# Kernel optimization log

Measured on AMD Instinct MI355X. Metric: run time of the kernel, lower is better.

Reference implementation:

```python
import jax, jax.numpy as jnp
import numpy as np

N_TOKENS = 8192
D_MODEL = 1024
D_HIDDEN = 2 * D_MODEL
N_EXPERTS = 16
TOP_K = 2


def setup_inputs() -> dict:
    key = jax.random.key(0)
    ks = jax.random.split(key, 6)
    s_in = 1.0 / np.sqrt(D_MODEL)
    s_hid = 1.0 / np.sqrt(D_HIDDEN)
    return {
        "x": jax.random.normal(ks[0], (N_TOKENS, D_MODEL), dtype=jnp.float32),
        # gate: Linear(d_model, n_experts, bias=False); stored as [E, d] like torch weight
        "Wg": jax.random.uniform(ks[1], (N_EXPERTS, D_MODEL), jnp.float32, -s_in, s_in),
        # per-expert MLP params, stacked on leading expert axis; W laid out [in, out]
        "W1": jax.random.uniform(ks[2], (N_EXPERTS, D_MODEL, D_HIDDEN), jnp.float32, -s_in, s_in),
        "b1": jax.random.uniform(ks[3], (N_EXPERTS, D_HIDDEN), jnp.float32, -s_in, s_in),
        "W2": jax.random.uniform(ks[4], (N_EXPERTS, D_HIDDEN, D_MODEL), jnp.float32, -s_hid, s_hid),
        "b2": jax.random.uniform(ks[5], (N_EXPERTS, D_MODEL), jnp.float32, -s_hid, s_hid),
    }


def reference(x, Wg, W1, b1, W2, b2):
    # Router: top-k logits, softmax over the k selected logits (in fp32)
    logits = x @ Wg.T                                  # [N, E]
    topk_vals, topk_idx = jax.lax.top_k(logits, TOP_K)  # [N, K]
    rw = jax.nn.softmax(topk_vals.astype(jnp.float32), axis=-1).astype(x.dtype)
    # Combine top-k weights into per-(token, expert) weights [N, E]
    cw = (jax.nn.one_hot(topk_idx, N_EXPERTS, dtype=x.dtype) * rw[..., None]).sum(axis=1)
    # Dense per-expert MLP, weighted combine (equivalent to gather/scatter index_add_)
    out = jnp.zeros_like(x)
    for e in range(N_EXPERTS):
        h = jax.nn.relu(x @ W1[e] + b1[e])             # [N, D_HIDDEN]
        out = out + (h @ W2[e] + b2[e]) * cw[:, e:e + 1]
    return out
```

## Files before the change

kernel.cpp:

```cpp
#include <hip/hip_runtime.h>
#include <hip/hip_bf16.h>
#include <stdint.h>

#define NTOK 8192
#define DM   1024
#define DH   2048
#define NE   16

#define NWRK  768
#define QCAP1 2048
#define QCAP2 1024

typedef float  f32x4  __attribute__((ext_vector_type(4)));
typedef __bf16 bf16x8 __attribute__((ext_vector_type(8)));

__device__ __forceinline__ unsigned short f2bf(float f) {
  union { __bf16 b; unsigned short u; } c; c.b = (__bf16)f; return c.u;
}

__device__ __forceinline__ void glds16(const void* g, void* l) {
  __builtin_amdgcn_global_load_lds(
      (const __attribute__((address_space(1))) void*)g,
      (__attribute__((address_space(3))) void*)l, 16, 0, 0);
}

__global__ __launch_bounds__(256) void router_kernel(
    const float* __restrict__ x, const float* __restrict__ Wg,
    unsigned short* __restrict__ xb, int* __restrict__ eidx,
    float* __restrict__ ewt, float* __restrict__ outz)
{
  const int lane = threadIdx.x & 63;
  const int wave = threadIdx.x >> 6;
  const int t = blockIdx.x * 4 + wave;
  const float* xr = x + (size_t)t * DM;

  float4 xv[4];
#pragma unroll
  for (int c = 0; c < 4; ++c)
    xv[c] = *(const float4*)(xr + c * 256 + lane * 4);

  unsigned short* xbr = xb + (size_t)t * DM;
#pragma unroll
  for (int c = 0; c < 4; ++c) {
    ushort4 u;
    u.x = f2bf(xv[c].x); u.y = f2bf(xv[c].y);
    u.z = f2bf(xv[c].z); u.w = f2bf(xv[c].w);
    *(ushort4*)(xbr + c * 256 + lane * 4) = u;
  }

  {
    float4 z4 = {0.f, 0.f, 0.f, 0.f};
    float* orow = outz + (size_t)t * DM;
#pragma unroll
    for (int c = 0; c < 4; ++c)
      *(float4*)(orow + c * 256 + lane * 4) = z4;
  }

  float acc[NE];
#pragma unroll
  for (int e = 0; e < NE; ++e) acc[e] = 0.f;
#pragma unroll
  for (int e = 0; e < NE; ++e) {
#pragma unroll
    for (int c = 0; c < 4; ++c) {
      float4 wv = *(const float4*)(Wg + e * DM + c * 256 + lane * 4);
      acc[e] += xv[c].x * wv.x + xv[c].y * wv.y + xv[c].z * wv.z + xv[c].w * wv.w;
    }
  }
#pragma unroll
  for (int e = 0; e < NE; ++e) {
    float v = acc[e];
    v += __shfl_xor(v, 1);  v += __shfl_xor(v, 2);  v += __shfl_xor(v, 4);
    v += __shfl_xor(v, 8);  v += __shfl_xor(v, 16); v += __shfl_xor(v, 32);
    acc[e] = v;
  }
  if (lane == 0) {
    float v0 = -1e30f; int i0 = 0;
#pragma unroll
    for (int e = 0; e < NE; ++e) if (acc[e] > v0) { v0 = acc[e]; i0 = e; }
    float v1 = -1e30f; int i1 = 0;
#pragma unroll
    for (int e = 0; e < NE; ++e) if (e != i0 && acc[e] > v1) { v1 = acc[e]; i1 = e; }
    float p = expf(v1 - v0);
    float s = 1.f / (1.f + p);
    eidx[2 * t] = i0; eidx[2 * t + 1] = i1;
    ewt[2 * t] = s;   ewt[2 * t + 1] = p * s;
  }
}

__global__ __launch_bounds__(1024) void planprep_kernel(
    const int* __restrict__ eidx, const float* __restrict__ ewt,
    int* __restrict__ cnt, int* __restrict__ offv,
    int* __restrict__ tok, float* __restrict__ wtl,
    int* __restrict__ wl1, int* __restrict__ wl2,
    int* __restrict__ qn1, int* __restrict__ qn2,
    int* __restrict__ qc1, int* __restrict__ qc2,
    const float* __restrict__ W1, unsigned short* __restrict__ w1t,
    const float* __restrict__ W2, unsigned short* __restrict__ w2t)
{
  __shared__ float t[4][64][68];
  __shared__ int wcnt[16][NE];
  __shared__ int wbase[16][NE];
  __shared__ int offs[NE];
  __shared__ int s_nmt[NE];
  __shared__ int s_pnmt[NE + 1];

  if (blockIdx.x != 0) {
    const int idx = blockIdx.x - 1;
    const int tg  = threadIdx.x >> 8;
    const int t8  = threadIdx.x & 255;
    const float* W; unsigned short* WT; int K, N, tt, bx, by;
    if (idx < 2048) {
      W = W1; WT = w1t; K = DM; N = DH;
      tt = idx * 4 + tg;
      int r = tt & 511; bx = r & 31; by = r >> 5;
    } else {
      W = W2; WT = w2t; K = DH; N = DM;
      tt = (idx - 2048) * 4 + tg;
      int r = tt & 511; bx = r & 15; by = r >> 4;
    }
    const int bz = tt >> 9;
    const int k0 = by * 64, n0 = bx * 64;
    const int tr = t8 >> 2;
    const int tc = (t8 & 3) * 16;
    const float* src = W + ((size_t)bz * K + k0) * N + n0;
#pragma unroll
    for (int j = 0; j < 4; ++j) {
      float4 v = *(const float4*)(src + (size_t)tr * N + tc + j * 4);
      t[tg][tc + j * 4 + 0][tr] = v.x;
      t[tg][tc + j * 4 + 1][tr] = v.y;
      t[tg][tc + j * 4 + 2][tr] = v.z;
      t[tg][tc + j * 4 + 3][tr] = v.w;
    }
    __syncthreads();
    unsigned short* dst = WT + ((size_t)bz * N + n0) * K + k0;
#pragma unroll
    for (int j = 0; j < 4; ++j) {
      float4 v = *(const float4*)(&t[tg][tr][tc + j * 4]);
      ushort4 u;
      u.x = f2bf(v.x); u.y = f2bf(v.y); u.z = f2bf(v.z); u.w = f2bf(v.w);
      *(ushort4*)(dst + (size_t)tr * K + tc + j * 4) = u;
    }
    return;
  }

  const int tid  = threadIdx.x;
  const int wave = tid >> 6;
  const int lane = tid & 63;
  const unsigned long long below = (1ull << lane) - 1ull;

  int   pe[16];
  float pw[16];
  int   count[NE];
#pragma unroll
  for (int e = 0; e < NE; ++e) count[e] = 0;
#pragma unroll
  for (int r = 0; r < 16; ++r) {
    int p = wave * 1024 + r * 64 + lane;
    pe[r] = eidx[p];
    pw[r] = ewt[p];
#pragma unroll
    for (int e = 0; e < NE; ++e) {
      unsigned long long m = __ballot(pe[r] == e);
      count[e] += (int)__popcll(m);
    }
  }
  if (lane == 0) {
#pragma unroll
    for (int e = 0; e < NE; ++e) wcnt[wave][e] = count[e];
  }
  __syncthreads();

  if (tid == 0) {
    int s = 0;
    s_pnmt[0] = 0;
    for (int e = 0; e < NE; ++e) {
      offs[e] = s;
      int tcnt = 0;
      for (int w = 0; w < 16; ++w) { wbase[w][e] = tcnt; tcnt += wcnt[w][e]; }
      cnt[e] = tcnt; offv[e] = s; s += tcnt;
      int nmt = (tcnt + 127) >> 7;
      s_nmt[e] = nmt;
      s_pnmt[e + 1] = s_pnmt[e] + nmt;
    }
    offv[NE] = s;
  }
  __syncthreads();

  if (tid < 8) {
    qn1[tid] = (s_nmt[tid] + s_nmt[tid + 8]) * 16;
    qn2[tid] = (s_nmt[tid] + s_nmt[tid + 8]) * 8;
    qc1[tid] = 0;
    qc2[tid] = 0;
  }

  {
    const int totmt = s_pnmt[NE];
    const int T1 = totmt * 16;
    for (int i = tid; i < T1; i += 1024) {
      int gmt = i >> 4, p = i & 15;
      int e = 0;
      while (s_pnmt[e + 1] <= gmt) ++e;
      int mt  = gmt - s_pnmt[e];
      int nmt = s_nmt[e];
      int h0  = (nmt + 1) >> 1;
      int pos_e = (mt < h0) ? (p * h0 + mt)
                            : (h0 * 16 + p * (nmt - h0) + (mt - h0));
      int xx   = e & 7;
      int base = (e < 8) ? 0 : s_nmt[e - 8] * 16;
      wl1[xx * QCAP1 + base + pos_e] = (e << 16) | (mt << 8) | p;
    }
    const int T2 = totmt * 8;
    for (int i = tid; i < T2; i += 1024) {
      int gmt = i >> 3, p = i & 7;
      int e = 0;
      while (s_pnmt[e + 1] <= gmt) ++e;
      int mt  = gmt - s_pnmt[e];
      int nmt = s_nmt[e];
      int h0  = (nmt + 1) >> 1;
      int pos_e = (mt < h0) ? (p * h0 + mt)
                            : (h0 * 8 + p * (nmt - h0) + (mt - h0));
      int xx   = e & 7;
      int base = (e < 8) ? 0 : s_nmt[e - 8] * 8;
      wl2[xx * QCAP2 + base + pos_e] = (e << 16) | (mt << 8) | p;
    }
  }

  int run[NE];
#pragma unroll
  for (int e = 0; e < NE; ++e) run[e] = 0;
#pragma unroll
  for (int r = 0; r < 16; ++r) {
    int p = wave * 1024 + r * 64 + lane;
#pragma unroll
    for (int e = 0; e < NE; ++e) {
      unsigned long long m = __ballot(pe[r] == e);
      if (pe[r] == e) {
        int rank = (int)__popcll(m & below);
        int slot = offs[e] + wbase[wave][e] + run[e] + rank;
        tok[slot] = p >> 1;
        wtl[slot] = pw[r];
      }
      run[e] += (int)__popcll(m);
    }
  }
}

template<int GATHER, int EPI, int KDIM, int NDIM, int QCAP>
__global__ __launch_bounds__(256, 3) void gemm_kernel(
    const unsigned short* __restrict__ Abase,
    const unsigned short* __restrict__ BT,
    const float* __restrict__ bias,
    const int* __restrict__ cnt, const int* __restrict__ offv,
    const int* __restrict__ tok, const float* __restrict__ wtl,
    const int* __restrict__ wl, const int* __restrict__ qn,
    int* __restrict__ qc, void* __restrict__ outp)
{
  __shared__ unsigned short Al[128 * 64];
  __shared__ unsigned short Bl[128 * 64];
  __shared__ int s_j;

  const int xcd = blockIdx.x & 7;
  const int* q_ = wl + xcd * QCAP;
  const int myqn = qn[xcd];

  const int tid  = threadIdx.x;
  const int lane = tid & 63;
  const int wave = tid >> 6;
  const int wr = wave >> 1;
  const int wc = wave & 1;

  const int lr = lane >> 3;
  const int lc = lane & 7;
  const int sc = (lc ^ lr) * 8;
  const int qq   = lane >> 4;
  const int ln15 = lane & 15;
  const int swz  = ln15 & 7;

  for (;;) {
    if (tid == 0) s_j = atomicAdd(&qc[xcd], 1);
    __syncthreads();
    const int j = s_j;
    if (j >= myqn) return;
    const int v = q_[j];

    const int e  = (v >> 16) & 0xff;
    const int m0 = ((v >> 8) & 0xff) * 128;
    const int n0 = (v & 0xff) * 128;
    const int count = cnt[e];
    const int o     = offv[e];

    const unsigned short* aptr[4];
    const unsigned short* bptr[4];
#pragma unroll
    for (int ii = 0; ii < 4; ++ii) {
      int i = wave * 4 + ii;
      int r = i * 8 + lr;
      int m = m0 + r; if (m > count - 1) m = count - 1;
      size_t arow = GATHER ? (size_t)tok[o + m] : (size_t)(o + m);
      aptr[ii] = Abase + arow * KDIM + sc;
      bptr[ii] = BT + ((size_t)e * NDIM + n0 + r) * KDIM + sc;
    }

    f32x4 acc[4][4];
#pragma unroll
    for (int a = 0; a < 4; ++a)
#pragma unroll
      for (int b = 0; b < 4; ++b) acc[a][b] = 0.f;

    for (int k0 = 0; k0 < KDIM; k0 += 64) {
#pragma unroll
      for (int ii = 0; ii < 4; ++ii) {
        int i = wave * 4 + ii;
        glds16(aptr[ii] + k0, &Al[i * 512]);
        glds16(bptr[ii] + k0, &Bl[i * 512]);
      }
      __syncthreads();
#pragma unroll
      for (int kk = 0; kk < 2; ++kk) {
        bf16x8 af[4], bg[4];
        const int ch = (kk * 4 + qq) ^ swz;
#pragma unroll
        for (int a = 0; a < 4; ++a) {
          int r = wr * 64 + a * 16 + ln15;
          af[a] = *(const bf16x8*)(&Al[r * 64 + ch * 8]);
        }
#pragma unroll
        for (int b = 0; b < 4; ++b) {
          int r = wc * 64 + b * 16 + ln15;
          bg[b] = *(const bf16x8*)(&Bl[r * 64 + ch * 8]);
        }
#pragma unroll
        for (int a = 0; a < 4; ++a)
#pragma unroll
          for (int b = 0; b < 4; ++b)
            acc[a][b] = __builtin_amdgcn_mfma_f32_16x16x32_bf16(af[a], bg[b], acc[a][b], 0, 0, 0);
      }
      __syncthreads();
    }

    float bn[4];
#pragma unroll
    for (int b = 0; b < 4; ++b)
      bn[b] = bias[(size_t)e * NDIM + n0 + wc * 64 + b * 16 + ln15];

    if (EPI == 0) {
      unsigned short* hout = (unsigned short*)outp;
#pragma unroll
      for (int a = 0; a < 4; ++a)
#pragma unroll
        for (int rg = 0; rg < 4; ++rg) {
          int r = wr * 64 + a * 16 + qq * 4 + rg;
          int m = m0 + r;
          if (m < count) {
            size_t slot = (size_t)(o + m);
#pragma unroll
            for (int b = 0; b < 4; ++b) {
              float v2 = acc[a][b][rg] + bn[b];
              v2 = v2 > 0.f ? v2 : 0.f;
              hout[slot * NDIM + n0 + wc * 64 + b * 16 + ln15] = f2bf(v2);
            }
          }
        }
    } else {
      float* obase = (float*)outp;
#pragma unroll
      for (int a = 0; a < 4; ++a)
#pragma unroll
        for (int rg = 0; rg < 4; ++rg) {
          int r = wr * 64 + a * 16 + qq * 4 + rg;
          int m = m0 + r;
          if (m < count) {
            int slot = o + m;
            int tk = tok[slot];
            float w = wtl[slot];
#pragma unroll
            for (int b = 0; b < 4; ++b) {
              float v2 = (acc[a][b][rg] + bn[b]) * w;
              atomicAdd(&obase[(size_t)tk * NDIM + n0 + wc * 64 + b * 16 + ln15], v2);
            }
          }
        }
    }
  }
}

extern "C" void kernel_launch(void* const* d_in, const int* in_sizes, int n_in,
                              void* d_out, int out_size, void* d_ws, size_t ws_size,
                              hipStream_t stream) {
  const float* x  = (const float*)d_in[0];
  const float* Wg = (const float*)d_in[1];
  const float* W1 = (const float*)d_in[2];
  const float* b1 = (const float*)d_in[3];
  const float* W2 = (const float*)d_in[4];
  const float* b2 = (const float*)d_in[5];

  constexpr size_t OFF_CNT  = 0;
  constexpr size_t OFF_OFF  = 256;
  constexpr size_t OFF_QN1  = 512;
  constexpr size_t OFF_QN2  = 544;
  constexpr size_t OFF_QC1  = 576;
  constexpr size_t OFF_QC2  = 608;
  constexpr size_t OFF_WL1  = 4096;
  constexpr size_t OFF_WL2  = OFF_WL1 + (size_t)8 * QCAP1 * 4;
  constexpr size_t OFF_EIDX = OFF_WL2 + (size_t)8 * QCAP2 * 4;
  constexpr size_t OFF_EWT  = OFF_EIDX + (size_t)NTOK * 2 * 4;
  constexpr size_t OFF_TOK  = OFF_EWT  + (size_t)NTOK * 2 * 4;
  constexpr size_t OFF_WTL  = OFF_TOK  + (size_t)NTOK * 2 * 4;
  constexpr size_t OFF_XB   = (size_t)1 << 20;
  constexpr size_t OFF_W1T  = OFF_XB  + (size_t)NTOK * DM * 2;
  constexpr size_t OFF_W2T  = OFF_W1T + (size_t)NE * DM * DH * 2;
  constexpr size_t OFF_H    = OFF_W2T + (size_t)NE * DH * DM * 2;
  constexpr size_t REQ      = OFF_H   + (size_t)NTOK * 2 * DH * 2;
  static_assert(OFF_WTL + (size_t)NTOK * 2 * 4 <= OFF_XB, "ws layout overlap");

  if (ws_size < REQ) {
    hipMemsetAsync(d_out, 0, (size_t)out_size * 4, stream);
    return;
  }

  char* ws = (char*)d_ws;
  int*   cnt    = (int*)(ws + OFF_CNT);
  int*   offv   = (int*)(ws + OFF_OFF);
  int*   qn1    = (int*)(ws + OFF_QN1);
  int*   qn2    = (int*)(ws + OFF_QN2);
  int*   qc1    = (int*)(ws + OFF_QC1);
  int*   qc2    = (int*)(ws + OFF_QC2);
  int*   wl1    = (int*)(ws + OFF_WL1);
  int*   wl2    = (int*)(ws + OFF_WL2);
  int*   eidx   = (int*)(ws + OFF_EIDX);
  float* ewt    = (float*)(ws + OFF_EWT);
  int*   tok    = (int*)(ws + OFF_TOK);
  float* wtl    = (float*)(ws + OFF_WTL);
  unsigned short* xb   = (unsigned short*)(ws + OFF_XB);
  unsigned short* w1t  = (unsigned short*)(ws + OFF_W1T);
  unsigned short* w2t  = (unsigned short*)(ws + OFF_W2T);
  unsigned short* hbuf = (unsigned short*)(ws + OFF_H);

  router_kernel<<<NTOK / 4, 256, 0, stream>>>(x, Wg, xb, eidx, ewt,
                                              (float*)d_out);
  planprep_kernel<<<4097, 1024, 0, stream>>>(
      eidx, ewt, cnt, offv, tok, wtl, wl1, wl2, qn1, qn2, qc1, qc2,
      W1, w1t, W2, w2t);

  gemm_kernel<1, 0, DM, DH, QCAP1><<<NWRK, 256, 0, stream>>>(
      xb, w1t, b1, cnt, offv, tok, wtl, wl1, qn1, qc1, hbuf);
  gemm_kernel<0, 1, DH, DM, QCAP2><<<NWRK, 256, 0, stream>>>(
      hbuf, w2t, b2, cnt, offv, tok, wtl, wl2, qn2, qc2, (float*)d_out);
}
```

Measured before the change: 344.1 us.

## Enlarge GEMM tiles to 256 rows, double-buffer LDS, add cross-XCD work stealing

Both grouped GEMMs move to 512-thread blocks with 256-row M tiles (256x256 for the first GEMM, 256x128 for the second). The K loop now double-buffers the LDS staging so the next k-slice loads while the current one feeds the MFMAs. Workers also steal from other XCD queues once their own queue is empty, and the persistent grid is smaller. The aim is more operand reuse, fewer weight reloads and hidden load latency, at the cost of much more LDS and register pressure, lower occupancy, and more padding waste on partial 256-row expert tiles.

```diff
diff --git a/kernel.cpp b/kernel.cpp
--- a/kernel.cpp
+++ b/kernel.cpp
@@ -7,8 +7,8 @@
 #define DH   2048
 #define NE   16
 
-#define NWRK  768
-#define QCAP1 2048
+#define NWRK  256
+#define QCAP1 1024
 #define QCAP2 1024
 
 typedef float  f32x4  __attribute__((ext_vector_type(4)));
@@ -179,7 +179,7 @@
       int tcnt = 0;
       for (int w = 0; w < 16; ++w) { wbase[w][e] = tcnt; tcnt += wcnt[w][e]; }
       cnt[e] = tcnt; offv[e] = s; s += tcnt;
-      int nmt = (tcnt + 127) >> 7;
+      int nmt = (tcnt + 255) >> 8;
       s_nmt[e] = nmt;
       s_pnmt[e + 1] = s_pnmt[e] + nmt;
     }
@@ -188,7 +188,7 @@
   __syncthreads();
 
   if (tid < 8) {
-    qn1[tid] = (s_nmt[tid] + s_nmt[tid + 8]) * 16;
+    qn1[tid] = (s_nmt[tid] + s_nmt[tid + 8]) * 8;
     qn2[tid] = (s_nmt[tid] + s_nmt[tid + 8]) * 8;
     qc1[tid] = 0;
     qc2[tid] = 0;
@@ -196,22 +196,8 @@
 
   {
     const int totmt = s_pnmt[NE];
-    const int T1 = totmt * 16;
-    for (int i = tid; i < T1; i += 1024) {
-      int gmt = i >> 4, p = i & 15;
-      int e = 0;
-      while (s_pnmt[e + 1] <= gmt) ++e;
-      int mt  = gmt - s_pnmt[e];
-      int nmt = s_nmt[e];
-      int h0  = (nmt + 1) >> 1;
-      int pos_e = (mt < h0) ? (p * h0 + mt)
-                            : (h0 * 16 + p * (nmt - h0) + (mt - h0));
-      int xx   = e & 7;
-      int base = (e < 8) ? 0 : s_nmt[e - 8] * 16;
-      wl1[xx * QCAP1 + base + pos_e] = (e << 16) | (mt << 8) | p;
-    }
-    const int T2 = totmt * 8;
-    for (int i = tid; i < T2; i += 1024) {
+    const int T = totmt * 8;
+    for (int i = tid; i < T; i += 1024) {
       int gmt = i >> 3, p = i & 7;
       int e = 0;
       while (s_pnmt[e + 1] <= gmt) ++e;
@@ -222,7 +208,9 @@
                             : (h0 * 8 + p * (nmt - h0) + (mt - h0));
       int xx   = e & 7;
       int base = (e < 8) ? 0 : s_nmt[e - 8] * 8;
-      wl2[xx * QCAP2 + base + pos_e] = (e << 16) | (mt << 8) | p;
+      int item = (e << 16) | (mt << 8) | p;
+      wl1[xx * QCAP1 + base + pos_e] = item;
+      wl2[xx * QCAP2 + base + pos_e] = item;
     }
   }
 
@@ -246,8 +234,8 @@
   }
 }
 
-template<int GATHER, int EPI, int KDIM, int NDIM, int QCAP>
-__global__ __launch_bounds__(256, 3) void gemm_kernel(
+template<int GATHER, int EPI, int BN, int NWN, int KDIM, int NDIM, int QCAP>
+__global__ __launch_bounds__(512, 2) void gemm_kernel(
     const unsigned short* __restrict__ Abase,
     const unsigned short* __restrict__ BT,
     const float* __restrict__ bias,
@@ -256,120 +244,141 @@
     const int* __restrict__ wl, const int* __restrict__ qn,
     int* __restrict__ qc, void* __restrict__ outp)
 {
-  __shared__ unsigned short Al[128 * 64];
-  __shared__ unsigned short Bl[128 * 64];
-  __shared__ int s_j;
-
-  const int xcd = blockIdx.x & 7;
-  const int* q_ = wl + xcd * QCAP;
-  const int myqn = qn[xcd];
-
+  constexpr int NWM   = 8 / NWN;
+  constexpr int WROWS = 256 / NWM;
+  constexpr int AR    = WROWS / 16;
+  constexpr int BI    = BN / 64;
+  constexpr int NT    = KDIM / 64;
+
+  __shared__ unsigned short Al[2][256 * 64];
+  __shared__ unsigned short Bl[2][BN * 64];
+  __shared__ int s_item;
+
+  const int xcd0 = blockIdx.x & 7;
   const int tid  = threadIdx.x;
   const int lane = tid & 63;
   const int wave = tid >> 6;
-  const int wr = wave >> 1;
-  const int wc = wave & 1;
+  const int wm = wave / NWN;
+  const int wn = wave % NWN;
 
   const int lr = lane >> 3;
   const int lc = lane & 7;
   const int sc = (lc ^ lr) * 8;
-  const int qq   = lane >> 4;
+  const int q    = lane >> 4;
   const int ln15 = lane & 15;
   const int swz  = ln15 & 7;
 
+  int sx = 0;
   for (;;) {
-    if (tid == 0) s_j = atomicAdd(&qc[xcd], 1);
+    if (tid == 0) {
+      int it = -1;
+      while (sx < 8) {
+        int x = (xcd0 + sx) & 7;
+        int jj = atomicAdd(&qc[x], 1);
+        if (jj < qn[x]) { it = wl[x * QCAP + jj]; break; }
+        ++sx;
+      }
+      s_item = it;
+    }
     __syncthreads();
-    const int j = s_j;
-    if (j >= myqn) return;
-    const int v = q_[j];
+    const int v = s_item;
+    if (v < 0) return;
 
     const int e  = (v >> 16) & 0xff;
-    const int m0 = ((v >> 8) & 0xff) * 128;
-    const int n0 = (v & 0xff) * 128;
+    const int m0 = ((v >> 8) & 0xff) * 256;
+    const int n0 = (v & 0xff) * BN;
     const int count = cnt[e];
     const int o     = offv[e];
 
     const unsigned short* aptr[4];
-    const unsigned short* bptr[4];
+    const unsigned short* bptr[BI];
 #pragma unroll
     for (int ii = 0; ii < 4; ++ii) {
-      int i = wave * 4 + ii;
-      int r = i * 8 + lr;
+      int r = ii * 64 + wave * 8 + lr;
       int m = m0 + r; if (m > count - 1) m = count - 1;
       size_t arow = GATHER ? (size_t)tok[o + m] : (size_t)(o + m);
       aptr[ii] = Abase + arow * KDIM + sc;
+    }
+#pragma unroll
+    for (int ii = 0; ii < BI; ++ii) {
+      int r = ii * 64 + wave * 8 + lr;
       bptr[ii] = BT + ((size_t)e * NDIM + n0 + r) * KDIM + sc;
     }
 
-    f32x4 acc[4][4];
-#pragma unroll
-    for (int a = 0; a < 4; ++a)
+    f32x4 acc[AR][4];
+#pragma unroll
+    for (int a = 0; a < AR; ++a)
 #pragma unroll
       for (int b = 0; b < 4; ++b) acc[a][b] = 0.f;
 
-    for (int k0 = 0; k0 < KDIM; k0 += 64) {
-#pragma unroll
-      for (int ii = 0; ii < 4; ++ii) {
-        int i = wave * 4 + ii;
-        glds16(aptr[ii] + k0, &Al[i * 512]);
-        glds16(bptr[ii] + k0, &Bl[i * 512]);
+#pragma unroll
+    for (int ii = 0; ii < 4; ++ii)
+      glds16(aptr[ii], &Al[0][(ii * 64 + wave * 8) * 64]);
+#pragma unroll
+    for (int ii = 0; ii < BI; ++ii)
+      glds16(bptr[ii], &Bl[0][(ii * 64 + wave * 8) * 64]);
+    __syncthreads();
+
+    int cur = 0;
+    for (int t = 0; t < NT; ++t) {
+      if (t + 1 < NT) {
+        const int k0 = (t + 1) * 64;
+#pragma unroll
+        for (int ii = 0; ii < 4; ++ii)
+          glds16(aptr[ii] + k0, &Al[cur ^ 1][(ii * 64 + wave * 8) * 64]);
+#pragma unroll
+        for (int ii = 0; ii < BI; ++ii)
+          glds16(bptr[ii] + k0, &Bl[cur ^ 1][(ii * 64 + wave * 8) * 64]);
       }
-      __syncthreads();
 #pragma unroll
       for (int kk = 0; kk < 2; ++kk) {
-        bf16x8 af[4], bg[4];
-        const int ch = (kk * 4 + qq) ^ swz;
-#pragma unroll
-        for (int a = 0; a < 4; ++a) {
-          int r = wr * 64 + a * 16 + ln15;
-          af[a] = *(const bf16x8*)(&Al[r * 64 + ch * 8]);
-        }
-#pragma unroll
-        for (int b = 0; b < 4; ++b) {
-          int r = wc * 64 + b * 16 + ln15;
-          bg[b] = *(const bf16x8*)(&Bl[r * 64 + ch * 8]);
-        }
-#pragma unroll
-        for (int a = 0; a < 4; ++a)
+        bf16x8 af[AR], bg[4];
+        const int ch = ((kk * 4 + q) ^ swz) * 8;
+#pragma unroll
+        for (int a = 0; a < AR; ++a)
+          af[a] = *(const bf16x8*)(&Al[cur][(wm * WROWS + a * 16 + ln15) * 64 + ch]);
+#pragma unroll
+        for (int b = 0; b < 4; ++b)
+          bg[b] = *(const bf16x8*)(&Bl[cur][(wn * 64 + b * 16 + ln15) * 64 + ch]);
+#pragma unroll
+        for (int a = 0; a < AR; ++a)
 #pragma unroll
           for (int b = 0; b < 4; ++b)
             acc[a][b] = __builtin_amdgcn_mfma_f32_16x16x32_bf16(af[a], bg[b], acc[a][b], 0, 0, 0);
       }
       __syncthreads();
+      cur ^= 1;
     }
 
     float bn[4];
 #pragma unroll
     for (int b = 0; b < 4; ++b)
-      bn[b] = bias[(size_t)e * NDIM + n0 + wc * 64 + b * 16 + ln15];
+      bn[b] = bias[(size_t)e * NDIM + n0 + wn * 64 + b * 16 + ln15];
 
     if (EPI == 0) {
       unsigned short* hout = (unsigned short*)outp;
 #pragma unroll
-      for (int a = 0; a < 4; ++a)
+      for (int a = 0; a < AR; ++a)
 #pragma unroll
         for (int rg = 0; rg < 4; ++rg) {
-          int r = wr * 64 + a * 16 + qq * 4 + rg;
-          int m = m0 + r;
+          int m = m0 + wm * WROWS + a * 16 + q * 4 + rg;
           if (m < count) {
             size_t slot = (size_t)(o + m);
 #pragma unroll
             for (int b = 0; b < 4; ++b) {
               float v2 = acc[a][b][rg] + bn[b];
               v2 = v2 > 0.f ? v2 : 0.f;
-              hout[slot * NDIM + n0 + wc * 64 + b * 16 + ln15] = f2bf(v2);
+              hout[slot * NDIM + n0 + wn * 64 + b * 16 + ln15] = f2bf(v2);
             }
           }
         }
     } else {
       float* obase = (float*)outp;
 #pragma unroll
-      for (int a = 0; a < 4; ++a)
+      for (int a = 0; a < AR; ++a)
 #pragma unroll
         for (int rg = 0; rg < 4; ++rg) {
-          int r = wr * 64 + a * 16 + qq * 4 + rg;
-          int m = m0 + r;
+          int m = m0 + wm * WROWS + a * 16 + q * 4 + rg;
           if (m < count) {
             int slot = o + m;
             int tk = tok[slot];
@@ -377,7 +386,7 @@
 #pragma unroll
             for (int b = 0; b < 4; ++b) {
               float v2 = (acc[a][b][rg] + bn[b]) * w;
-              atomicAdd(&obase[(size_t)tk * NDIM + n0 + wc * 64 + b * 16 + ln15], v2);
+              atomicAdd(&obase[(size_t)tk * NDIM + n0 + wn * 64 + b * 16 + ln15], v2);
             }
           }
         }
@@ -443,8 +452,8 @@
       eidx, ewt, cnt, offv, tok, wtl, wl1, wl2, qn1, qn2, qc1, qc2,
       W1, w1t, W2, w2t);
 
-  gemm_kernel<1, 0, DM, DH, QCAP1><<<NWRK, 256, 0, stream>>>(
+  gemm_kernel<1, 0, 256, 4, DM, DH, QCAP1><<<NWRK, 512, 0, stream>>>(
       xb, w1t, b1, cnt, offv, tok, wtl, wl1, qn1, qc1, hbuf);
-  gemm_kernel<0, 1, DH, DM, QCAP2><<<NWRK, 256, 0, stream>>>(
+  gemm_kernel<0, 1, 128, 2, DH, DM, QCAP2><<<NWRK, 512, 0, stream>>>(
       hbuf, w2t, b2, cnt, offv, tok, wtl, wl2, qn2, qc2, (float*)d_out);
 }
```

Result: slower. 504.5 us (+46.6%).

## Fuse router into plan/prep kernel with atomic completion flag

Applied to the files above, without the earlier changes.

Merges the separate router kernel into the plan/weight-transpose kernel as 512 extra blocks of 16 tokens each. Each router block bumps a global done counter after a threadfence. Block 0 spins on that counter before building the expert plan, and reads the routing results with atomic loads. This removes one kernel boundary and lets routing overlap with the weight transpose, at the cost of an extra memset launch and a spin-wait that assumes the router blocks get scheduled.

```diff
diff --git a/kernel.cpp b/kernel.cpp
--- a/kernel.cpp
+++ b/kernel.cpp
@@ -10,6 +10,7 @@
 #define NWRK  768
 #define QCAP1 2048
 #define QCAP2 1024
+#define NRTB  512
 
 typedef float  f32x4  __attribute__((ext_vector_type(4)));
 typedef __bf16 bf16x8 __attribute__((ext_vector_type(8)));
@@ -24,79 +25,18 @@
       (__attribute__((address_space(3))) void*)l, 16, 0, 0);
 }
 
-__global__ __launch_bounds__(256) void router_kernel(
+__global__ __launch_bounds__(1024) void prep_kernel(
     const float* __restrict__ x, const float* __restrict__ Wg,
     unsigned short* __restrict__ xb, int* __restrict__ eidx,
-    float* __restrict__ ewt, float* __restrict__ outz)
-{
-  const int lane = threadIdx.x & 63;
-  const int wave = threadIdx.x >> 6;
-  const int t = blockIdx.x * 4 + wave;
-  const float* xr = x + (size_t)t * DM;
-
-  float4 xv[4];
-#pragma unroll
-  for (int c = 0; c < 4; ++c)
-    xv[c] = *(const float4*)(xr + c * 256 + lane * 4);
-
-  unsigned short* xbr = xb + (size_t)t * DM;
-#pragma unroll
-  for (int c = 0; c < 4; ++c) {
-    ushort4 u;
-    u.x = f2bf(xv[c].x); u.y = f2bf(xv[c].y);
-    u.z = f2bf(xv[c].z); u.w = f2bf(xv[c].w);
-    *(ushort4*)(xbr + c * 256 + lane * 4) = u;
-  }
-
-  {
-    float4 z4 = {0.f, 0.f, 0.f, 0.f};
-    float* orow = outz + (size_t)t * DM;
-#pragma unroll
-    for (int c = 0; c < 4; ++c)
-      *(float4*)(orow + c * 256 + lane * 4) = z4;
-  }
-
-  float acc[NE];
-#pragma unroll
-  for (int e = 0; e < NE; ++e) acc[e] = 0.f;
-#pragma unroll
-  for (int e = 0; e < NE; ++e) {
-#pragma unroll
-    for (int c = 0; c < 4; ++c) {
-      float4 wv = *(const float4*)(Wg + e * DM + c * 256 + lane * 4);
-      acc[e] += xv[c].x * wv.x + xv[c].y * wv.y + xv[c].z * wv.z + xv[c].w * wv.w;
-    }
-  }
-#pragma unroll
-  for (int e = 0; e < NE; ++e) {
-    float v = acc[e];
-    v += __shfl_xor(v, 1);  v += __shfl_xor(v, 2);  v += __shfl_xor(v, 4);
-    v += __shfl_xor(v, 8);  v += __shfl_xor(v, 16); v += __shfl_xor(v, 32);
-    acc[e] = v;
-  }
-  if (lane == 0) {
-    float v0 = -1e30f; int i0 = 0;
-#pragma unroll
-    for (int e = 0; e < NE; ++e) if (acc[e] > v0) { v0 = acc[e]; i0 = e; }
-    float v1 = -1e30f; int i1 = 0;
-#pragma unroll
-    for (int e = 0; e < NE; ++e) if (e != i0 && acc[e] > v1) { v1 = acc[e]; i1 = e; }
-    float p = expf(v1 - v0);
-    float s = 1.f / (1.f + p);
-    eidx[2 * t] = i0; eidx[2 * t + 1] = i1;
-    ewt[2 * t] = s;   ewt[2 * t + 1] = p * s;
-  }
-}
-
-__global__ __launch_bounds__(1024) void planprep_kernel(
-    const int* __restrict__ eidx, const float* __restrict__ ewt,
+    float* __restrict__ ewt, float* __restrict__ outz,
     int* __restrict__ cnt, int* __restrict__ offv,
     int* __restrict__ tok, float* __restrict__ wtl,
     int* __restrict__ wl1, int* __restrict__ wl2,
     int* __restrict__ qn1, int* __restrict__ qn2,
     int* __restrict__ qc1, int* __restrict__ qc2,
     const float* __restrict__ W1, unsigned short* __restrict__ w1t,
-    const float* __restrict__ W2, unsigned short* __restrict__ w2t)
+    const float* __restrict__ W2, unsigned short* __restrict__ w2t,
+    int* __restrict__ done)
 {
   __shared__ float t[4][64][68];
   __shared__ int wcnt[16][NE];
@@ -105,10 +45,13 @@
   __shared__ int s_nmt[NE];
   __shared__ int s_pnmt[NE + 1];
 
-  if (blockIdx.x != 0) {
-    const int idx = blockIdx.x - 1;
-    const int tg  = threadIdx.x >> 8;
-    const int t8  = threadIdx.x & 255;
+  const int bid = blockIdx.x;
+  const int tid = threadIdx.x;
+
+  if (bid >= 1 + NRTB) {
+    const int idx = bid - 1 - NRTB;
+    const int tg  = tid >> 8;
+    const int t8  = tid & 255;
     const float* W; unsigned short* WT; int K, N, tt, bx, by;
     if (idx < 2048) {
       W = W1; WT = w1t; K = DM; N = DH;
@@ -144,7 +87,77 @@
     return;
   }
 
-  const int tid  = threadIdx.x;
+  if (bid >= 1) {
+    const int lane = tid & 63;
+    const int wave = tid >> 6;
+    const int tk = (bid - 1) * 16 + wave;
+    const float* xr = x + (size_t)tk * DM;
+
+    float4 xv[4];
+#pragma unroll
+    for (int c = 0; c < 4; ++c)
+      xv[c] = *(const float4*)(xr + c * 256 + lane * 4);
+
+    unsigned short* xbr = xb + (size_t)tk * DM;
+#pragma unroll
+    for (int c = 0; c < 4; ++c) {
+      ushort4 u;
+      u.x = f2bf(xv[c].x); u.y = f2bf(xv[c].y);
+      u.z = f2bf(xv[c].z); u.w = f2bf(xv[c].w);
+      *(ushort4*)(xbr + c * 256 + lane * 4) = u;
+    }
+
+    {
+      float4 z4 = {0.f, 0.f, 0.f, 0.f};
+      float* orow = outz + (size_t)tk * DM;
+#pragma unroll
+      for (int c = 0; c < 4; ++c)
+        *(float4*)(orow + c * 256 + lane * 4) = z4;
+    }
+
+    float acc[NE];
+#pragma unroll
+    for (int e = 0; e < NE; ++e) acc[e] = 0.f;
+#pragma unroll
+    for (int e = 0; e < NE; ++e) {
+#pragma unroll
+      for (int c = 0; c < 4; ++c) {
+        float4 wv = *(const float4*)(Wg + e * DM + c * 256 + lane * 4);
+        acc[e] += xv[c].x * wv.x + xv[c].y * wv.y + xv[c].z * wv.z + xv[c].w * wv.w;
+      }
+    }
+#pragma unroll
+    for (int e = 0; e < NE; ++e) {
+      float v = acc[e];
+      v += __shfl_xor(v, 1);  v += __shfl_xor(v, 2);  v += __shfl_xor(v, 4);
+      v += __shfl_xor(v, 8);  v += __shfl_xor(v, 16); v += __shfl_xor(v, 32);
+      acc[e] = v;
+    }
+    if (lane == 0) {
+      float v0 = -1e30f; int i0 = 0;
+#pragma unroll
+      for (int e = 0; e < NE; ++e) if (acc[e] > v0) { v0 = acc[e]; i0 = e; }
+      float v1 = -1e30f; int i1 = 0;
+#pragma unroll
+      for (int e = 0; e < NE; ++e) if (e != i0 && acc[e] > v1) { v1 = acc[e]; i1 = e; }
+      float p = expf(v1 - v0);
+      float s = 1.f / (1.f + p);
+      eidx[2 * tk] = i0; eidx[2 * tk + 1] = i1;
+      ewt[2 * tk] = s;   ewt[2 * tk + 1] = p * s;
+    }
+    __threadfence();
+    __syncthreads();
+    if (tid == 0) atomicAdd(done, 1);
+    return;
+  }
+
+  if (tid == 0) {
+    while (__hip_atomic_load(done, __ATOMIC_ACQUIRE,
+                             __HIP_MEMORY_SCOPE_AGENT) < NRTB)
+      __builtin_amdgcn_s_sleep(32);
+  }
+  __syncthreads();
+
   const int wave = tid >> 6;
   const int lane = tid & 63;
   const unsigned long long below = (1ull << lane) - 1ull;
@@ -157,8 +170,10 @@
 #pragma unroll
   for (int r = 0; r < 16; ++r) {
     int p = wave * 1024 + r * 64 + lane;
-    pe[r] = eidx[p];
-    pw[r] = ewt[p];
+    pe[r] = __hip_atomic_load(&eidx[p], __ATOMIC_RELAXED,
+                              __HIP_MEMORY_SCOPE_AGENT);
+    pw[r] = __hip_atomic_load(&ewt[p], __ATOMIC_RELAXED,
+                              __HIP_MEMORY_SCOPE_AGENT);
 #pragma unroll
     for (int e = 0; e < NE; ++e) {
       unsigned long long m = __ballot(pe[r] == e);
@@ -401,6 +416,7 @@
   constexpr size_t OFF_QN2  = 544;
   constexpr size_t OFF_QC1  = 576;
   constexpr size_t OFF_QC2  = 608;
+  constexpr size_t OFF_FLAG = 768;
   constexpr size_t OFF_WL1  = 4096;
   constexpr size_t OFF_WL2  = OFF_WL1 + (size_t)8 * QCAP1 * 4;
   constexpr size_t OFF_EIDX = OFF_WL2 + (size_t)8 * QCAP2 * 4;
@@ -426,6 +442,7 @@
   int*   qn2    = (int*)(ws + OFF_QN2);
   int*   qc1    = (int*)(ws + OFF_QC1);
   int*   qc2    = (int*)(ws + OFF_QC2);
+  int*   flag   = (int*)(ws + OFF_FLAG);
   int*   wl1    = (int*)(ws + OFF_WL1);
   int*   wl2    = (int*)(ws + OFF_WL2);
   int*   eidx   = (int*)(ws + OFF_EIDX);
@@ -437,11 +454,12 @@
   unsigned short* w2t  = (unsigned short*)(ws + OFF_W2T);
   unsigned short* hbuf = (unsigned short*)(ws + OFF_H);
 
-  router_kernel<<<NTOK / 4, 256, 0, stream>>>(x, Wg, xb, eidx, ewt,
-                                              (float*)d_out);
-  planprep_kernel<<<4097, 1024, 0, stream>>>(
-      eidx, ewt, cnt, offv, tok, wtl, wl1, wl2, qn1, qn2, qc1, qc2,
-      W1, w1t, W2, w2t);
+  hipMemsetAsync(flag, 0, 4, stream);
+
+  prep_kernel<<<1 + NRTB + 4096, 1024, 0, stream>>>(
+      x, Wg, xb, eidx, ewt, (float*)d_out,
+      cnt, offv, tok, wtl, wl1, wl2, qn1, qn2, qc1, qc2,
+      W1, w1t, W2, w2t, flag);
 
   gemm_kernel<1, 0, DM, DH, QCAP1><<<NWRK, 256, 0, stream>>>(
       xb, w1t, b1, cnt, offv, tok, wtl, wl1, qn1, qc1, hbuf);
```

New measurement: 613.5 us. 78.3% more time.
